# Kernel tuning notes

Hardware: AMD Instinct MI355X
Metric: run time of the kernel (lower is better)

The kernel has to match this reference:

```python
import jax, jax.numpy as jnp
import numpy as np

B, N, D, H = 4, 512, 4, 256


def _linear_params(key, fan_in, fan_out):
    # torch.nn.Linear default init: U(-1/sqrt(fan_in), 1/sqrt(fan_in))
    lim = 1.0 / np.sqrt(fan_in)
    kw, kb = jax.random.split(key)
    W = jax.random.uniform(kw, (fan_in, fan_out), minval=-lim, maxval=lim, dtype=jnp.float32)
    b = jax.random.uniform(kb, (fan_out,), minval=-lim, maxval=lim, dtype=jnp.float32)
    return W, b


def setup_inputs() -> dict:
    key = jax.random.key(0)
    ks = jax.random.split(key, 8)
    x = jax.random.normal(ks[0], (B, N, D), dtype=jnp.float32)
    adj = jax.random.uniform(ks[1], (B, N, N), dtype=jnp.float32)  # soft adjacency in [0,1)
    W_e1, b_e1 = _linear_params(ks[2], 2 * D, H)
    W_e2, b_e2 = _linear_params(ks[3], H, H)
    W_n1, b_n1 = _linear_params(ks[4], H, H)
    W_n2, b_n2 = _linear_params(ks[5], H, H)
    W_o1, b_o1 = _linear_params(ks[6], D + H, H)
    W_o, b_o = _linear_params(ks[7], H, D)
    return {
        "x": x, "adj": adj,
        "W_e1": W_e1, "b_e1": b_e1, "W_e2": W_e2, "b_e2": b_e2,
        "W_n1": W_n1, "b_n1": b_n1, "W_n2": W_n2, "b_n2": b_n2,
        "W_o1": W_o1, "b_o1": b_o1, "W_o": W_o, "b_o": b_o,
    }


def reference(x, adj, W_e1, b_e1, W_e2, b_e2, W_n1, b_n1, W_n2, b_n2, W_o1, b_o1, W_o, b_o):
    b_, n_, d_ = x.shape
    # innode[b,i,j,:] = x[b,j]; outnode[b,i,j,:] = x[b,i]
    innode = jnp.broadcast_to(x[:, None, :, :], (b_, n_, n_, d_))
    outnode = jnp.broadcast_to(x[:, :, None, :], (b_, n_, n_, d_))
    edge_in = jnp.concatenate([innode, outnode], axis=-1)          # [B,N,N,2D]
    node2edge = jax.nn.relu(edge_in @ W_e1 + b_e1)                 # [B,N,N,H]
    edge2edge = jax.nn.relu(node2edge @ W_e2 + b_e2)               # [B,N,N,H]
    # adjacency-masked sum over axis 1 (the i axis)
    agg = jnp.einsum('bij,bijh->bjh', adj, edge2edge)              # [B,N,H]
    out1 = jax.nn.relu(agg @ W_n1 + b_n1)
    out2 = jax.nn.relu(out1 @ W_n2 + b_n2)
    out3 = jnp.concatenate([x, out2], axis=-1)                     # [B,N,D+H]
    out4 = out3 @ W_o1 + b_o1
    out5 = out4 @ W_o + b_o                                        # [B,N,D]
    # CONTINUOUS is False for the classifier variant
    return jax.nn.log_softmax(out5, axis=2)
```

## Files before the change

kernel.cpp:

```cpp
#include <hip/hip_runtime.h>
#include <hip/hip_fp16.h>
#include <math.h>

#define Bq 4
#define Nq 512
#define Dq 4
#define Hq 256

typedef _Float16 f16x8 __attribute__((ext_vector_type(8)));
typedef float f32x4 __attribute__((ext_vector_type(4)));

__device__ __forceinline__ f16x8 hadd_relu(f16x8 u, f16x8 v) {
    f16x8 s = u + v;
    const f16x8 z = (f16x8)(_Float16)0.0f;
    return __builtin_elementwise_max(s, z);
}

__global__ __launch_bounds__(256) void prep_uv(
    const float* __restrict__ x, const float* __restrict__ We1,
    const float* __restrict__ be1, __half* __restrict__ U, __half* __restrict__ V) {
    const int bn = blockIdx.x;
    const int k = threadIdx.x;
    const float* xp = x + bn * Dq;
    const float x0 = xp[0], x1 = xp[1], x2 = xp[2], x3 = xp[3];
    float u = be1[k];
    u = fmaf(x0, We1[0 * 256 + k], u);
    u = fmaf(x1, We1[1 * 256 + k], u);
    u = fmaf(x2, We1[2 * 256 + k], u);
    u = fmaf(x3, We1[3 * 256 + k], u);
    float v = x0 * We1[4 * 256 + k];
    v = fmaf(x1, We1[5 * 256 + k], v);
    v = fmaf(x2, We1[6 * 256 + k], v);
    v = fmaf(x3, We1[7 * 256 + k], v);
    U[(size_t)bn * Hq + k] = __float2half(u);
    V[(size_t)bn * Hq + k] = __float2half(v);
}

__global__ __launch_bounds__(256, 2) void edge_gemm(
    const __half* __restrict__ U, const __half* __restrict__ V,
    const float* __restrict__ We2, const float* __restrict__ be2,
    const float* __restrict__ adj, float* __restrict__ aggws) {
    __shared__ __align__(16) char smem[59392];
    __half* Wt = (__half*)smem;
    __half* Us = (__half*)(smem + 32768);
    __half* Vs = (__half*)(smem + 40960);
    float* adjs = (float*)(smem + 57344);
    float* red = (float*)(smem + 40960);

    const int bid = blockIdx.x;
    const int hq_ = bid & 3;
    const int jt = (bid >> 2) & 31;
    const int b = bid >> 7;
    const int h_base = hq_ * 64;
    const int j_base = jt * 16;
    const int t = threadIdx.x;
    const int lane = t & 63;
    const int w = t >> 6;
    const int q = lane >> 4;
    const int l15 = lane & 15;

    const __half* Vb = V + (size_t)b * Nq * Hq;
    const float* adjb = adj + (size_t)b * Nq * Nq;

    const int srow = t >> 4;
    const int sc0 = (t & 15) * 2;

    {
        const int n = t & 63;
        const int swz = n & 31;
        for (int kk = (t >> 6); kk < 256; kk += 4) {
            float val = We2[kk * 256 + h_base + n];
            Wt[n * 256 + ((((kk >> 3) ^ swz)) << 3) + (kk & 7)] = __float2half(val);
        }
    }
    {
        const uint4* gp = (const uint4*)(U + (size_t)(b * Nq + j_base + srow) * Hq);
        uint4 v0 = gp[sc0];
        uint4 v1 = gp[sc0 + 1];
        *(uint4*)&Us[srow * 256 + ((sc0 ^ srow) << 3)] = v0;
        *(uint4*)&Us[srow * 256 + (((sc0 + 1) ^ srow) << 3)] = v1;
    }

    float bias[4];
#pragma unroll
    for (int nt = 0; nt < 4; ++nt) bias[nt] = be2[h_base + nt * 16 + l15];

    f32x4 agg[4];
#pragma unroll
    for (int nt = 0; nt < 4; ++nt) agg[nt] = (f32x4){0.f, 0.f, 0.f, 0.f};

    uint4 pva, pvb; float pad_;
    {
        const uint4* gp = (const uint4*)(Vb + (size_t)(0 + srow) * Hq);
        pva = gp[sc0]; pvb = gp[sc0 + 1];
        pad_ = adjb[(size_t)(0 + srow) * Nq + j_base + (t & 15)];
        *(uint4*)&Vs[0 * 4096 + srow * 256 + ((sc0 ^ srow) << 3)] = pva;
        *(uint4*)&Vs[0 * 4096 + srow * 256 + (((sc0 + 1) ^ srow) << 3)] = pvb;
        adjs[0 * 256 + t] = pad_;
    }
    {
        const uint4* gp = (const uint4*)(Vb + (size_t)(16 + srow) * Hq);
        pva = gp[sc0]; pvb = gp[sc0 + 1];
        pad_ = adjb[(size_t)(16 + srow) * Nq + j_base + (t & 15)];
    }
    __syncthreads();

    for (int ch = 0; ch < 32; ++ch) {
        const int cur = ch & 1;
        const __half* Vcur = Vs + cur * 4096;
        const float* Acur = adjs + cur * 256;

        f32x4 acc[4][4];
#pragma unroll
        for (int mi = 0; mi < 4; ++mi)
#pragma unroll
            for (int nt = 0; nt < 4; ++nt)
                acc[mi][nt] = (f32x4){bias[nt], bias[nt], bias[nt], bias[nt]};

#pragma unroll
        for (int ks = 0; ks < 8; ++ks) {
            const int c = ks * 4 + q;
            const f16x8 uvec = *(const f16x8*)&Us[l15 * 256 + ((c ^ l15) << 3)];
            f16x8 afrag[4];
#pragma unroll
            for (int mi = 0; mi < 4; ++mi) {
                const int iv = w * 4 + mi;
                const f16x8 vvec = *(const f16x8*)&Vcur[iv * 256 + ((c ^ iv) << 3)];
                afrag[mi] = hadd_relu(uvec, vvec);
            }
            f16x8 bf[4];
#pragma unroll
            for (int nt = 0; nt < 4; ++nt) {
                const int rn = nt * 16 + l15;
                bf[nt] = *(const f16x8*)&Wt[rn * 256 + ((c ^ (rn & 31)) << 3)];
            }
#pragma unroll
            for (int mi = 0; mi < 4; ++mi)
#pragma unroll
                for (int nt = 0; nt < 4; ++nt)
                    acc[mi][nt] = __builtin_amdgcn_mfma_f32_16x16x32_f16(
                        afrag[mi], bf[nt], acc[mi][nt], 0, 0, 0);
        }

#pragma unroll
        for (int mi = 0; mi < 4; ++mi) {
            const int iv = w * 4 + mi;
            const f32x4 av = *(const f32x4*)&Acur[iv * 16 + q * 4];
#pragma unroll
            for (int nt = 0; nt < 4; ++nt) {
                agg[nt][0] = fmaf(av[0], fmaxf(acc[mi][nt][0], 0.f), agg[nt][0]);
                agg[nt][1] = fmaf(av[1], fmaxf(acc[mi][nt][1], 0.f), agg[nt][1]);
                agg[nt][2] = fmaf(av[2], fmaxf(acc[mi][nt][2], 0.f), agg[nt][2]);
                agg[nt][3] = fmaf(av[3], fmaxf(acc[mi][nt][3], 0.f), agg[nt][3]);
            }
        }

        if (ch < 31) {
            const int nxt = cur ^ 1;
            *(uint4*)&Vs[nxt * 4096 + srow * 256 + ((sc0 ^ srow) << 3)] = pva;
            *(uint4*)&Vs[nxt * 4096 + srow * 256 + (((sc0 + 1) ^ srow) << 3)] = pvb;
            adjs[nxt * 256 + t] = pad_;
            if (ch < 30) {
                const int i_base = (ch + 2) * 16;
                const uint4* gp = (const uint4*)(Vb + (size_t)(i_base + srow) * Hq);
                pva = gp[sc0]; pvb = gp[sc0 + 1];
                pad_ = adjb[(size_t)(i_base + srow) * Nq + j_base + (t & 15)];
            }
        }
        __syncthreads();
    }

#pragma unroll
    for (int nt = 0; nt < 4; ++nt)
#pragma unroll
        for (int r = 0; r < 4; ++r)
            red[w * 1024 + (q * 4 + r) * 64 + nt * 16 + l15] = agg[nt][r];
    __syncthreads();
    {
        const int j = t >> 4;
        const int h0 = (t & 15) * 4;
        f32x4 s = *(const f32x4*)&red[0 * 1024 + j * 64 + h0];
        s += *(const f32x4*)&red[1 * 1024 + j * 64 + h0];
        s += *(const f32x4*)&red[2 * 1024 + j * 64 + h0];
        s += *(const f32x4*)&red[3 * 1024 + j * 64 + h0];
        *(f32x4*)&aggws[(size_t)(b * Nq + j_base + j) * Hq + h_base + h0] = s;
    }
}

__global__ __launch_bounds__(256) void tail_kernel(
    const float* __restrict__ aggws, const float* __restrict__ x,
    const float* __restrict__ Wn1, const float* __restrict__ bn1,
    const float* __restrict__ Wn2, const float* __restrict__ bn2,
    const float* __restrict__ Wo1, const float* __restrict__ bo1,
    const float* __restrict__ Wo, const float* __restrict__ bo,
    float* __restrict__ out) {
    __shared__ __align__(16) float bufA[256 * 4];
    __shared__ __align__(16) float bufB[256 * 4];
    __shared__ float xs[4][4];
    __shared__ float s5[4][4];
    const int bid = blockIdx.x;
    const int b = bid >> 7;
    const int n0 = (bid & 127) * 4;
    const int t = threadIdx.x;

#pragma unroll
    for (int ni = 0; ni < 4; ++ni)
        bufA[t * 4 + ni] = aggws[(size_t)(b * Nq + n0 + ni) * Hq + t];
    if (t < 16) xs[t >> 2][t & 3] = x[(size_t)(b * Nq + n0 + (t >> 2)) * Dq + (t & 3)];
    __syncthreads();

    float c0, c1, c2, c3;
    c0 = c1 = c2 = c3 = bn1[t];
#pragma unroll 8
    for (int k = 0; k < 256; ++k) {
        const float wv = Wn1[k * 256 + t];
        const float4 av = *(const float4*)&bufA[k * 4];
        c0 = fmaf(av.x, wv, c0); c1 = fmaf(av.y, wv, c1);
        c2 = fmaf(av.z, wv, c2); c3 = fmaf(av.w, wv, c3);
    }
    bufB[t * 4 + 0] = fmaxf(c0, 0.f); bufB[t * 4 + 1] = fmaxf(c1, 0.f);
    bufB[t * 4 + 2] = fmaxf(c2, 0.f); bufB[t * 4 + 3] = fmaxf(c3, 0.f);
    __syncthreads();

    c0 = c1 = c2 = c3 = bn2[t];
#pragma unroll 8
    for (int k = 0; k < 256; ++k) {
        const float wv = Wn2[k * 256 + t];
        const float4 av = *(const float4*)&bufB[k * 4];
        c0 = fmaf(av.x, wv, c0); c1 = fmaf(av.y, wv, c1);
        c2 = fmaf(av.z, wv, c2); c3 = fmaf(av.w, wv, c3);
    }
    bufA[t * 4 + 0] = fmaxf(c0, 0.f); bufA[t * 4 + 1] = fmaxf(c1, 0.f);
    bufA[t * 4 + 2] = fmaxf(c2, 0.f); bufA[t * 4 + 3] = fmaxf(c3, 0.f);
    __syncthreads();

    c0 = c1 = c2 = c3 = bo1[t];
#pragma unroll
    for (int d = 0; d < 4; ++d) {
        const float wv = Wo1[d * 256 + t];
        c0 = fmaf(xs[0][d], wv, c0); c1 = fmaf(xs[1][d], wv, c1);
        c2 = fmaf(xs[2][d], wv, c2); c3 = fmaf(xs[3][d], wv, c3);
    }
#pragma unroll 8
    for (int k = 0; k < 256; ++k) {
        const float wv = Wo1[(4 + k) * 256 + t];
        const float4 av = *(const float4*)&bufA[k * 4];
        c0 = fmaf(av.x, wv, c0); c1 = fmaf(av.y, wv, c1);
        c2 = fmaf(av.z, wv, c2); c3 = fmaf(av.w, wv, c3);
    }
    bufB[t * 4 + 0] = c0; bufB[t * 4 + 1] = c1;
    bufB[t * 4 + 2] = c2; bufB[t * 4 + 3] = c3;
    __syncthreads();

    const int d = t >> 6;
    const int lane = t & 63;
    float p0 = 0.f, p1 = 0.f, p2 = 0.f, p3 = 0.f;
    for (int k = lane; k < 256; k += 64) {
        const float wv = Wo[k * 4 + d];
        const float4 av = *(const float4*)&bufB[k * 4];
        p0 = fmaf(av.x, wv, p0); p1 = fmaf(av.y, wv, p1);
        p2 = fmaf(av.z, wv, p2); p3 = fmaf(av.w, wv, p3);
    }
#pragma unroll
    for (int off = 32; off > 0; off >>= 1) {
        p0 += __shfl_down(p0, off); p1 += __shfl_down(p1, off);
        p2 += __shfl_down(p2, off); p3 += __shfl_down(p3, off);
    }
    if (lane == 0) {
        s5[0][d] = p0 + bo[d]; s5[1][d] = p1 + bo[d];
        s5[2][d] = p2 + bo[d]; s5[3][d] = p3 + bo[d];
    }
    __syncthreads();
    if (t < 4) {
        const float v0 = s5[t][0], v1 = s5[t][1], v2 = s5[t][2], v3 = s5[t][3];
        const float m = fmaxf(fmaxf(v0, v1), fmaxf(v2, v3));
        const float s = expf(v0 - m) + expf(v1 - m) + expf(v2 - m) + expf(v3 - m);
        const float lse = m + logf(s);
        float* op = out + (size_t)(b * Nq + n0 + t) * Dq;
        op[0] = v0 - lse; op[1] = v1 - lse; op[2] = v2 - lse; op[3] = v3 - lse;
    }
}

extern "C" void kernel_launch(void* const* d_in, const int* in_sizes, int n_in,
                              void* d_out, int out_size, void* d_ws, size_t ws_size,
                              hipStream_t stream) {
    const float* x   = (const float*)d_in[0];
    const float* adj = (const float*)d_in[1];
    const float* We1 = (const float*)d_in[2];
    const float* be1 = (const float*)d_in[3];
    const float* We2 = (const float*)d_in[4];
    const float* be2 = (const float*)d_in[5];
    const float* Wn1 = (const float*)d_in[6];
    const float* bn1 = (const float*)d_in[7];
    const float* Wn2 = (const float*)d_in[8];
    const float* bn2 = (const float*)d_in[9];
    const float* Wo1 = (const float*)d_in[10];
    const float* bo1 = (const float*)d_in[11];
    const float* Wo  = (const float*)d_in[12];
    const float* bo  = (const float*)d_in[13];
    float* out = (float*)d_out;

    __half* U = (__half*)d_ws;
    __half* V = U + (size_t)Bq * Nq * Hq;
    float* aggws = (float*)((char*)d_ws + (size_t)2 * Bq * Nq * Hq * sizeof(__half));

    prep_uv<<<Bq * Nq, 256, 0, stream>>>(x, We1, be1, U, V);
    edge_gemm<<<512, 256, 0, stream>>>(U, V, We2, be2, adj, aggws);
    tail_kernel<<<512, 256, 0, stream>>>(aggws, x, Wn1, bn1, Wn2, bn2, Wo1, bo1, Wo, bo, out);
}
```

Baseline: 242.9 us.

## Split edge GEMM over i halves, keep U in registers, raise occupancy

The edge GEMM kernel now splits the i-reduction into two halves, doubling the grid to 1024 blocks. Each half writes its partial aggregate to a separate workspace slice, and the tail kernel sums the two slices. U fragments are held in registers instead of shared memory, which shrinks LDS use so launch bounds can request 3 blocks per SM. The aim is better occupancy and load balance across the CUs. The cost is twice the W staging per block, more registers per thread, and an extra partial-sum read in the tail.

```diff
diff --git a/kernel.cpp b/kernel.cpp
--- a/kernel.cpp
+++ b/kernel.cpp
@@ -36,23 +36,24 @@
     V[(size_t)bn * Hq + k] = __float2half(v);
 }
 
-__global__ __launch_bounds__(256, 2) void edge_gemm(
+__global__ __launch_bounds__(256, 3) void edge_gemm(
     const __half* __restrict__ U, const __half* __restrict__ V,
     const float* __restrict__ We2, const float* __restrict__ be2,
     const float* __restrict__ adj, float* __restrict__ aggws) {
-    __shared__ __align__(16) char smem[59392];
+    __shared__ __align__(16) char smem[51200];
     __half* Wt = (__half*)smem;
-    __half* Us = (__half*)(smem + 32768);
-    __half* Vs = (__half*)(smem + 40960);
-    float* adjs = (float*)(smem + 57344);
-    float* red = (float*)(smem + 40960);
+    __half* Vs = (__half*)(smem + 32768);
+    float* adjs = (float*)(smem + 49152);
+    float* red = (float*)(smem + 32768);
 
     const int bid = blockIdx.x;
     const int hq_ = bid & 3;
     const int jt = (bid >> 2) & 31;
-    const int b = bid >> 7;
+    const int ih = (bid >> 7) & 1;
+    const int b = bid >> 8;
     const int h_base = hq_ * 64;
     const int j_base = jt * 16;
+    const int i_first = ih * 256;
     const int t = threadIdx.x;
     const int lane = t & 63;
     const int w = t >> 6;
@@ -73,12 +74,12 @@
             Wt[n * 256 + ((((kk >> 3) ^ swz)) << 3) + (kk & 7)] = __float2half(val);
         }
     }
-    {
-        const uint4* gp = (const uint4*)(U + (size_t)(b * Nq + j_base + srow) * Hq);
-        uint4 v0 = gp[sc0];
-        uint4 v1 = gp[sc0 + 1];
-        *(uint4*)&Us[srow * 256 + ((sc0 ^ srow) << 3)] = v0;
-        *(uint4*)&Us[srow * 256 + (((sc0 + 1) ^ srow) << 3)] = v1;
+
+    f16x8 uvec[8];
+#pragma unroll
+    for (int ks = 0; ks < 8; ++ks) {
+        const int c = ks * 4 + q;
+        uvec[ks] = *(const f16x8*)&U[(size_t)(b * Nq + j_base + l15) * Hq + c * 8];
     }
 
     float bias[4];
@@ -91,21 +92,21 @@
 
     uint4 pva, pvb; float pad_;
     {
-        const uint4* gp = (const uint4*)(Vb + (size_t)(0 + srow) * Hq);
+        const uint4* gp = (const uint4*)(Vb + (size_t)(i_first + srow) * Hq);
         pva = gp[sc0]; pvb = gp[sc0 + 1];
-        pad_ = adjb[(size_t)(0 + srow) * Nq + j_base + (t & 15)];
+        pad_ = adjb[(size_t)(i_first + srow) * Nq + j_base + (t & 15)];
         *(uint4*)&Vs[0 * 4096 + srow * 256 + ((sc0 ^ srow) << 3)] = pva;
         *(uint4*)&Vs[0 * 4096 + srow * 256 + (((sc0 + 1) ^ srow) << 3)] = pvb;
         adjs[0 * 256 + t] = pad_;
     }
     {
-        const uint4* gp = (const uint4*)(Vb + (size_t)(16 + srow) * Hq);
+        const uint4* gp = (const uint4*)(Vb + (size_t)(i_first + 16 + srow) * Hq);
         pva = gp[sc0]; pvb = gp[sc0 + 1];
-        pad_ = adjb[(size_t)(16 + srow) * Nq + j_base + (t & 15)];
-    }
-    __syncthreads();
-
-    for (int ch = 0; ch < 32; ++ch) {
+        pad_ = adjb[(size_t)(i_first + 16 + srow) * Nq + j_base + (t & 15)];
+    }
+    __syncthreads();
+
+    for (int ch = 0; ch < 16; ++ch) {
         const int cur = ch & 1;
         const __half* Vcur = Vs + cur * 4096;
         const float* Acur = adjs + cur * 256;
@@ -120,13 +121,12 @@
 #pragma unroll
         for (int ks = 0; ks < 8; ++ks) {
             const int c = ks * 4 + q;
-            const f16x8 uvec = *(const f16x8*)&Us[l15 * 256 + ((c ^ l15) << 3)];
             f16x8 afrag[4];
 #pragma unroll
             for (int mi = 0; mi < 4; ++mi) {
                 const int iv = w * 4 + mi;
                 const f16x8 vvec = *(const f16x8*)&Vcur[iv * 256 + ((c ^ iv) << 3)];
-                afrag[mi] = hadd_relu(uvec, vvec);
+                afrag[mi] = hadd_relu(uvec[ks], vvec);
             }
             f16x8 bf[4];
 #pragma unroll
@@ -155,13 +155,13 @@
             }
         }
 
-        if (ch < 31) {
+        if (ch < 15) {
             const int nxt = cur ^ 1;
             *(uint4*)&Vs[nxt * 4096 + srow * 256 + ((sc0 ^ srow) << 3)] = pva;
             *(uint4*)&Vs[nxt * 4096 + srow * 256 + (((sc0 + 1) ^ srow) << 3)] = pvb;
             adjs[nxt * 256 + t] = pad_;
-            if (ch < 30) {
-                const int i_base = (ch + 2) * 16;
+            if (ch < 14) {
+                const int i_base = i_first + (ch + 2) * 16;
                 const uint4* gp = (const uint4*)(Vb + (size_t)(i_base + srow) * Hq);
                 pva = gp[sc0]; pvb = gp[sc0 + 1];
                 pad_ = adjb[(size_t)(i_base + srow) * Nq + j_base + (t & 15)];
@@ -183,7 +183,8 @@
         s += *(const f32x4*)&red[1 * 1024 + j * 64 + h0];
         s += *(const f32x4*)&red[2 * 1024 + j * 64 + h0];
         s += *(const f32x4*)&red[3 * 1024 + j * 64 + h0];
-        *(f32x4*)&aggws[(size_t)(b * Nq + j_base + j) * Hq + h_base + h0] = s;
+        float* aggp = aggws + (size_t)ih * Bq * Nq * Hq;
+        *(f32x4*)&aggp[(size_t)(b * Nq + j_base + j) * Hq + h_base + h0] = s;
     }
 }
 
@@ -203,9 +204,12 @@
     const int n0 = (bid & 127) * 4;
     const int t = threadIdx.x;
 
-#pragma unroll
-    for (int ni = 0; ni < 4; ++ni)
-        bufA[t * 4 + ni] = aggws[(size_t)(b * Nq + n0 + ni) * Hq + t];
+    const size_t half = (size_t)Bq * Nq * Hq;
+#pragma unroll
+    for (int ni = 0; ni < 4; ++ni) {
+        const size_t idx = (size_t)(b * Nq + n0 + ni) * Hq + t;
+        bufA[t * 4 + ni] = aggws[idx] + aggws[half + idx];
+    }
     if (t < 16) xs[t >> 2][t & 3] = x[(size_t)(b * Nq + n0 + (t >> 2)) * Dq + (t & 3)];
     __syncthreads();
 
@@ -305,6 +309,6 @@
     float* aggws = (float*)((char*)d_ws + (size_t)2 * Bq * Nq * Hq * sizeof(__half));
 
     prep_uv<<<Bq * Nq, 256, 0, stream>>>(x, We1, be1, U, V);
-    edge_gemm<<<512, 256, 0, stream>>>(U, V, We2, be2, adj, aggws);
+    edge_gemm<<<1024, 256, 0, stream>>>(U, V, We2, be2, adj, aggws);
     tail_kernel<<<512, 256, 0, stream>>>(aggws, x, Wn1, bn1, Wn2, bn2, Wo1, bo1, Wo, bo, out);
 }
```

New measurement: 536.0 us. 2.21x slower.

## Load V tiles directly into LDS asynchronously, double chunk size, widen tail rows

Applied to the files above, without the earlier changes.

The edge GEMM now streams V chunks straight from global memory into LDS with global_load_lds, instead of staging them through registers and doing swizzled LDS stores. Each chunk grows from 16 to 32 i-rows, which halves the number of barriers per block but doubles the accumulator registers. The LDS V tile is no longer XOR-swizzled, so bank conflicts may appear. Separately, the tail kernel handles 8 nodes per block instead of 4, reusing each weight load across more rows at the cost of half as many blocks.

```diff
diff --git a/kernel.cpp b/kernel.cpp
--- a/kernel.cpp
+++ b/kernel.cpp
@@ -14,6 +14,12 @@
     f16x8 s = u + v;
     const f16x8 z = (f16x8)(_Float16)0.0f;
     return __builtin_elementwise_max(s, z);
+}
+
+__device__ __forceinline__ void gl_lds16(const void* g, void* l) {
+    __builtin_amdgcn_global_load_lds(
+        (const __attribute__((address_space(1))) unsigned int*)g,
+        (__attribute__((address_space(3))) unsigned int*)l, 16, 0, 0);
 }
 
 __global__ __launch_bounds__(256) void prep_uv(
@@ -40,11 +46,11 @@
     const __half* __restrict__ U, const __half* __restrict__ V,
     const float* __restrict__ We2, const float* __restrict__ be2,
     const float* __restrict__ adj, float* __restrict__ aggws) {
-    __shared__ __align__(16) char smem[59392];
+    __shared__ __align__(16) char smem[77824];
     __half* Wt = (__half*)smem;
     __half* Us = (__half*)(smem + 32768);
     __half* Vs = (__half*)(smem + 40960);
-    float* adjs = (float*)(smem + 57344);
+    float* adjs = (float*)(smem + 73728);
     float* red = (float*)(smem + 40960);
 
     const int bid = blockIdx.x;
@@ -62,9 +68,6 @@
     const __half* Vb = V + (size_t)b * Nq * Hq;
     const float* adjb = adj + (size_t)b * Nq * Nq;
 
-    const int srow = t >> 4;
-    const int sc0 = (t & 15) * 2;
-
     {
         const int n = t & 63;
         const int swz = n & 31;
@@ -74,6 +77,8 @@
         }
     }
     {
+        const int srow = t >> 4;
+        const int sc0 = (t & 15) * 2;
         const uint4* gp = (const uint4*)(U + (size_t)(b * Nq + j_base + srow) * Hq);
         uint4 v0 = gp[sc0];
         uint4 v1 = gp[sc0 + 1];
@@ -89,30 +94,47 @@
 #pragma unroll
     for (int nt = 0; nt < 4; ++nt) agg[nt] = (f32x4){0.f, 0.f, 0.f, 0.f};
 
-    uint4 pva, pvb; float pad_;
+    const int r0 = t >> 4;
+    const int col = t & 15;
+
+#pragma unroll
+    for (int inst = 0; inst < 4; ++inst)
+        gl_lds16((const char*)Vb + (size_t)w * 4096 + inst * 1024 + lane * 16,
+                 Vs + w * 2048 + inst * 512);
     {
-        const uint4* gp = (const uint4*)(Vb + (size_t)(0 + srow) * Hq);
-        pva = gp[sc0]; pvb = gp[sc0 + 1];
-        pad_ = adjb[(size_t)(0 + srow) * Nq + j_base + (t & 15)];
-        *(uint4*)&Vs[0 * 4096 + srow * 256 + ((sc0 ^ srow) << 3)] = pva;
-        *(uint4*)&Vs[0 * 4096 + srow * 256 + (((sc0 + 1) ^ srow) << 3)] = pvb;
-        adjs[0 * 256 + t] = pad_;
-    }
-    {
-        const uint4* gp = (const uint4*)(Vb + (size_t)(16 + srow) * Hq);
-        pva = gp[sc0]; pvb = gp[sc0 + 1];
-        pad_ = adjb[(size_t)(16 + srow) * Nq + j_base + (t & 15)];
-    }
-    __syncthreads();
-
-    for (int ch = 0; ch < 32; ++ch) {
+        float a0 = adjb[(size_t)r0 * Nq + j_base + col];
+        float a1 = adjb[(size_t)(r0 + 16) * Nq + j_base + col];
+        adjs[t] = a0;
+        adjs[256 + t] = a1;
+    }
+    float pa0 = adjb[(size_t)(32 + r0) * Nq + j_base + col];
+    float pa1 = adjb[(size_t)(32 + r0 + 16) * Nq + j_base + col];
+    __syncthreads();
+
+    for (int ch = 0; ch < 16; ++ch) {
         const int cur = ch & 1;
-        const __half* Vcur = Vs + cur * 4096;
-        const float* Acur = adjs + cur * 256;
-
-        f32x4 acc[4][4];
-#pragma unroll
-        for (int mi = 0; mi < 4; ++mi)
+        const int nxt = cur ^ 1;
+        const __half* Vcur = Vs + cur * 8192;
+        const float* Acur = adjs + cur * 512;
+
+        if (ch < 15) {
+            const size_t goff = (size_t)(ch + 1) * 32 * 512;
+#pragma unroll
+            for (int inst = 0; inst < 4; ++inst)
+                gl_lds16((const char*)Vb + goff + (size_t)w * 4096 + inst * 1024 + lane * 16,
+                         Vs + nxt * 8192 + w * 2048 + inst * 512);
+            adjs[nxt * 512 + t] = pa0;
+            adjs[nxt * 512 + 256 + t] = pa1;
+            if (ch < 14) {
+                const int ib = (ch + 2) * 32;
+                pa0 = adjb[(size_t)(ib + r0) * Nq + j_base + col];
+                pa1 = adjb[(size_t)(ib + r0 + 16) * Nq + j_base + col];
+            }
+        }
+
+        f32x4 acc[8][4];
+#pragma unroll
+        for (int mi = 0; mi < 8; ++mi)
 #pragma unroll
             for (int nt = 0; nt < 4; ++nt)
                 acc[mi][nt] = (f32x4){bias[nt], bias[nt], bias[nt], bias[nt]};
@@ -121,13 +143,6 @@
         for (int ks = 0; ks < 8; ++ks) {
             const int c = ks * 4 + q;
             const f16x8 uvec = *(const f16x8*)&Us[l15 * 256 + ((c ^ l15) << 3)];
-            f16x8 afrag[4];
-#pragma unroll
-            for (int mi = 0; mi < 4; ++mi) {
-                const int iv = w * 4 + mi;
-                const f16x8 vvec = *(const f16x8*)&Vcur[iv * 256 + ((c ^ iv) << 3)];
-                afrag[mi] = hadd_relu(uvec, vvec);
-            }
             f16x8 bf[4];
 #pragma unroll
             for (int nt = 0; nt < 4; ++nt) {
@@ -135,16 +150,26 @@
                 bf[nt] = *(const f16x8*)&Wt[rn * 256 + ((c ^ (rn & 31)) << 3)];
             }
 #pragma unroll
-            for (int mi = 0; mi < 4; ++mi)
-#pragma unroll
-                for (int nt = 0; nt < 4; ++nt)
-                    acc[mi][nt] = __builtin_amdgcn_mfma_f32_16x16x32_f16(
-                        afrag[mi], bf[nt], acc[mi][nt], 0, 0, 0);
+            for (int g = 0; g < 2; ++g) {
+                f16x8 afrag[4];
+#pragma unroll
+                for (int m4 = 0; m4 < 4; ++m4) {
+                    const int iv = w * 8 + g * 4 + m4;
+                    const f16x8 vvec = *(const f16x8*)&Vcur[iv * 256 + c * 8];
+                    afrag[m4] = hadd_relu(uvec, vvec);
+                }
+#pragma unroll
+                for (int m4 = 0; m4 < 4; ++m4)
+#pragma unroll
+                    for (int nt = 0; nt < 4; ++nt)
+                        acc[g * 4 + m4][nt] = __builtin_amdgcn_mfma_f32_16x16x32_f16(
+                            afrag[m4], bf[nt], acc[g * 4 + m4][nt], 0, 0, 0);
+            }
         }
 
 #pragma unroll
-        for (int mi = 0; mi < 4; ++mi) {
-            const int iv = w * 4 + mi;
+        for (int mi = 0; mi < 8; ++mi) {
+            const int iv = w * 8 + mi;
             const f32x4 av = *(const f32x4*)&Acur[iv * 16 + q * 4];
 #pragma unroll
             for (int nt = 0; nt < 4; ++nt) {
@@ -152,19 +177,6 @@
                 agg[nt][1] = fmaf(av[1], fmaxf(acc[mi][nt][1], 0.f), agg[nt][1]);
                 agg[nt][2] = fmaf(av[2], fmaxf(acc[mi][nt][2], 0.f), agg[nt][2]);
                 agg[nt][3] = fmaf(av[3], fmaxf(acc[mi][nt][3], 0.f), agg[nt][3]);
-            }
-        }
-
-        if (ch < 31) {
-            const int nxt = cur ^ 1;
-            *(uint4*)&Vs[nxt * 4096 + srow * 256 + ((sc0 ^ srow) << 3)] = pva;
-            *(uint4*)&Vs[nxt * 4096 + srow * 256 + (((sc0 + 1) ^ srow) << 3)] = pvb;
-            adjs[nxt * 256 + t] = pad_;
-            if (ch < 30) {
-                const int i_base = (ch + 2) * 16;
-                const uint4* gp = (const uint4*)(Vb + (size_t)(i_base + srow) * Hq);
-                pva = gp[sc0]; pvb = gp[sc0 + 1];
-                pad_ = adjb[(size_t)(i_base + srow) * Nq + j_base + (t & 15)];
             }
         }
         __syncthreads();
@@ -194,84 +206,100 @@
     const float* __restrict__ Wo1, const float* __restrict__ bo1,
     const float* __restrict__ Wo, const float* __restrict__ bo,
     float* __restrict__ out) {
-    __shared__ __align__(16) float bufA[256 * 4];
-    __shared__ __align__(16) float bufB[256 * 4];
-    __shared__ float xs[4][4];
-    __shared__ float s5[4][4];
+    __shared__ __align__(16) float bufA[256 * 8];
+    __shared__ __align__(16) float bufB[256 * 8];
+    __shared__ float xs[8][4];
+    __shared__ float s5[8][4];
     const int bid = blockIdx.x;
-    const int b = bid >> 7;
-    const int n0 = (bid & 127) * 4;
+    const int b = bid >> 6;
+    const int n0 = (bid & 63) * 8;
     const int t = threadIdx.x;
 
 #pragma unroll
-    for (int ni = 0; ni < 4; ++ni)
-        bufA[t * 4 + ni] = aggws[(size_t)(b * Nq + n0 + ni) * Hq + t];
-    if (t < 16) xs[t >> 2][t & 3] = x[(size_t)(b * Nq + n0 + (t >> 2)) * Dq + (t & 3)];
-    __syncthreads();
-
-    float c0, c1, c2, c3;
-    c0 = c1 = c2 = c3 = bn1[t];
-#pragma unroll 8
+    for (int ni = 0; ni < 8; ++ni)
+        bufA[t * 8 + ni] = aggws[(size_t)(b * Nq + n0 + ni) * Hq + t];
+    if (t < 32) xs[t >> 2][t & 3] = x[(size_t)(b * Nq + n0 + (t >> 2)) * Dq + (t & 3)];
+    __syncthreads();
+
+    float c[8];
+#pragma unroll
+    for (int ni = 0; ni < 8; ++ni) c[ni] = bn1[t];
+#pragma unroll 4
     for (int k = 0; k < 256; ++k) {
         const float wv = Wn1[k * 256 + t];
-        const float4 av = *(const float4*)&bufA[k * 4];
-        c0 = fmaf(av.x, wv, c0); c1 = fmaf(av.y, wv, c1);
-        c2 = fmaf(av.z, wv, c2); c3 = fmaf(av.w, wv, c3);
-    }
-    bufB[t * 4 + 0] = fmaxf(c0, 0.f); bufB[t * 4 + 1] = fmaxf(c1, 0.f);
-    bufB[t * 4 + 2] = fmaxf(c2, 0.f); bufB[t * 4 + 3] = fmaxf(c3, 0.f);
-    __syncthreads();
-
-    c0 = c1 = c2 = c3 = bn2[t];
-#pragma unroll 8
+        const float4 a0 = *(const float4*)&bufA[k * 8];
+        const float4 a1 = *(const float4*)&bufA[k * 8 + 4];
+        c[0] = fmaf(a0.x, wv, c[0]); c[1] = fmaf(a0.y, wv, c[1]);
+        c[2] = fmaf(a0.z, wv, c[2]); c[3] = fmaf(a0.w, wv, c[3]);
+        c[4] = fmaf(a1.x, wv, c[4]); c[5] = fmaf(a1.y, wv, c[5]);
+        c[6] = fmaf(a1.z, wv, c[6]); c[7] = fmaf(a1.w, wv, c[7]);
+    }
+#pragma unroll
+    for (int ni = 0; ni < 8; ++ni) bufB[t * 8 + ni] = fmaxf(c[ni], 0.f);
+    __syncthreads();
+
+#pragma unroll
+    for (int ni = 0; ni < 8; ++ni) c[ni] = bn2[t];
+#pragma unroll 4
     for (int k = 0; k < 256; ++k) {
         const float wv = Wn2[k * 256 + t];
-        const float4 av = *(const float4*)&bufB[k * 4];
-        c0 = fmaf(av.x, wv, c0); c1 = fmaf(av.y, wv, c1);
-        c2 = fmaf(av.z, wv, c2); c3 = fmaf(av.w, wv, c3);
-    }
-    bufA[t * 4 + 0] = fmaxf(c0, 0.f); bufA[t * 4 + 1] = fmaxf(c1, 0.f);
-    bufA[t * 4 + 2] = fmaxf(c2, 0.f); bufA[t * 4 + 3] = fmaxf(c3, 0.f);
-    __syncthreads();
-
-    c0 = c1 = c2 = c3 = bo1[t];
+        const float4 a0 = *(const float4*)&bufB[k * 8];
+        const float4 a1 = *(const float4*)&bufB[k * 8 + 4];
+        c[0] = fmaf(a0.x, wv, c[0]); c[1] = fmaf(a0.y, wv, c[1]);
+        c[2] = fmaf(a0.z, wv, c[2]); c[3] = fmaf(a0.w, wv, c[3]);
+        c[4] = fmaf(a1.x, wv, c[4]); c[5] = fmaf(a1.y, wv, c[5]);
+        c[6] = fmaf(a1.z, wv, c[6]); c[7] = fmaf(a1.w, wv, c[7]);
+    }
+#pragma unroll
+    for (int ni = 0; ni < 8; ++ni) bufA[t * 8 + ni] = fmaxf(c[ni], 0.f);
+    __syncthreads();
+
+#pragma unroll
+    for (int ni = 0; ni < 8; ++ni) c[ni] = bo1[t];
 #pragma unroll
     for (int d = 0; d < 4; ++d) {
         const float wv = Wo1[d * 256 + t];
-        c0 = fmaf(xs[0][d], wv, c0); c1 = fmaf(xs[1][d], wv, c1);
-        c2 = fmaf(xs[2][d], wv, c2); c3 = fmaf(xs[3][d], wv, c3);
-    }
-#pragma unroll 8
+#pragma unroll
+        for (int ni = 0; ni < 8; ++ni) c[ni] = fmaf(xs[ni][d], wv, c[ni]);
+    }
+#pragma unroll 4
     for (int k = 0; k < 256; ++k) {
         const float wv = Wo1[(4 + k) * 256 + t];
-        const float4 av = *(const float4*)&bufA[k * 4];
-        c0 = fmaf(av.x, wv, c0); c1 = fmaf(av.y, wv, c1);
-        c2 = fmaf(av.z, wv, c2); c3 = fmaf(av.w, wv, c3);
-    }
-    bufB[t * 4 + 0] = c0; bufB[t * 4 + 1] = c1;
-    bufB[t * 4 + 2] = c2; bufB[t * 4 + 3] = c3;
+        const float4 a0 = *(const float4*)&bufA[k * 8];
+        const float4 a1 = *(const float4*)&bufA[k * 8 + 4];
+        c[0] = fmaf(a0.x, wv, c[0]); c[1] = fmaf(a0.y, wv, c[1]);
+        c[2] = fmaf(a0.z, wv, c[2]); c[3] = fmaf(a0.w, wv, c[3]);
+        c[4] = fmaf(a1.x, wv, c[4]); c[5] = fmaf(a1.y, wv, c[5]);
+        c[6] = fmaf(a1.z, wv, c[6]); c[7] = fmaf(a1.w, wv, c[7]);
+    }
+#pragma unroll
+    for (int ni = 0; ni < 8; ++ni) bufB[t * 8 + ni] = c[ni];
     __syncthreads();
 
     const int d = t >> 6;
     const int lane = t & 63;
-    float p0 = 0.f, p1 = 0.f, p2 = 0.f, p3 = 0.f;
+    float p[8];
+#pragma unroll
+    for (int ni = 0; ni < 8; ++ni) p[ni] = 0.f;
     for (int k = lane; k < 256; k += 64) {
         const float wv = Wo[k * 4 + d];
-        const float4 av = *(const float4*)&bufB[k * 4];
-        p0 = fmaf(av.x, wv, p0); p1 = fmaf(av.y, wv, p1);
-        p2 = fmaf(av.z, wv, p2); p3 = fmaf(av.w, wv, p3);
-    }
-#pragma unroll
-    for (int off = 32; off > 0; off >>= 1) {
-        p0 += __shfl_down(p0, off); p1 += __shfl_down(p1, off);
-        p2 += __shfl_down(p2, off); p3 += __shfl_down(p3, off);
-    }
+        const float4 a0 = *(const float4*)&bufB[k * 8];
+        const float4 a1 = *(const float4*)&bufB[k * 8 + 4];
+        p[0] = fmaf(a0.x, wv, p[0]); p[1] = fmaf(a0.y, wv, p[1]);
+        p[2] = fmaf(a0.z, wv, p[2]); p[3] = fmaf(a0.w, wv, p[3]);
+        p[4] = fmaf(a1.x, wv, p[4]); p[5] = fmaf(a1.y, wv, p[5]);
+        p[6] = fmaf(a1.z, wv, p[6]); p[7] = fmaf(a1.w, wv, p[7]);
+    }
+#pragma unroll
+    for (int off = 32; off > 0; off >>= 1)
+#pragma unroll
+        for (int ni = 0; ni < 8; ++ni) p[ni] += __shfl_down(p[ni], off);
     if (lane == 0) {
-        s5[0][d] = p0 + bo[d]; s5[1][d] = p1 + bo[d];
-        s5[2][d] = p2 + bo[d]; s5[3][d] = p3 + bo[d];
-    }
-    __syncthreads();
-    if (t < 4) {
+#pragma unroll
+        for (int ni = 0; ni < 8; ++ni) s5[ni][d] = p[ni] + bo[d];
+    }
+    __syncthreads();
+    if (t < 8) {
         const float v0 = s5[t][0], v1 = s5[t][1], v2 = s5[t][2], v3 = s5[t][3];
         const float m = fmaxf(fmaxf(v0, v1), fmaxf(v2, v3));
         const float s = expf(v0 - m) + expf(v1 - m) + expf(v2 - m) + expf(v3 - m);
@@ -306,5 +334,5 @@
 
     prep_uv<<<Bq * Nq, 256, 0, stream>>>(x, We1, be1, U, V);
     edge_gemm<<<512, 256, 0, stream>>>(U, V, We2, be2, adj, aggws);
-    tail_kernel<<<512, 256, 0, stream>>>(aggws, x, Wn1, bn1, Wn2, bn2, Wo1, bo1, Wo, bo, out);
-}
+    tail_kernel<<<256, 256, 0, stream>>>(aggws, x, Wn1, bn1, Wn2, bn2, Wo1, bo1, Wo, bo, out);
+}
```

Measured after the change: 283.8 us. 1.17x slower.

## Rewrite node MLP tail with fp16 MFMA over 64-row tiles

Applied to the files above, without the earlier changes.

Replaces the scalar fp32 tail kernel, which handled 4 nodes per block, with an MFMA-based version that handles 64 nodes per block using fp16 activations in swizzled shared memory. A new wprep kernel transposes and converts Wn1, Wn2 and Wo1 to fp16 each call. The goal is to stop re-streaming the 256x256 fp32 weights for every 4 nodes and to use matrix cores. In exchange it adds a kernel launch, lowers precision to fp16, and runs the tail on only 32 blocks, so much of the GPU sits idle.

```diff
diff --git a/kernel.cpp b/kernel.cpp
--- a/kernel.cpp
+++ b/kernel.cpp
@@ -14,6 +14,13 @@
     f16x8 s = u + v;
     const f16x8 z = (f16x8)(_Float16)0.0f;
     return __builtin_elementwise_max(s, z);
+}
+
+__device__ __forceinline__ uint4 cvt8h(const float* p) {
+    union { __half h[8]; uint4 u; } r;
+#pragma unroll
+    for (int i = 0; i < 8; ++i) r.h[i] = __float2half(p[i]);
+    return r.u;
 }
 
 __global__ __launch_bounds__(256) void prep_uv(
@@ -36,6 +43,16 @@
     V[(size_t)bn * Hq + k] = __float2half(v);
 }
 
+__global__ __launch_bounds__(256) void wprep(
+    const float* __restrict__ Wn1, const float* __restrict__ Wn2,
+    const float* __restrict__ Wo1, __half* __restrict__ Wt16) {
+    const int n = blockIdx.x & 255;
+    const int mat = blockIdx.x >> 8;
+    const int k = threadIdx.x;
+    const float* W = (mat == 0) ? Wn1 : (mat == 1) ? Wn2 : (Wo1 + 4 * 256);
+    Wt16[((size_t)mat * 256 + n) * 256 + k] = __float2half(W[k * 256 + n]);
+}
+
 __global__ __launch_bounds__(256, 2) void edge_gemm(
     const __half* __restrict__ U, const __half* __restrict__ V,
     const float* __restrict__ We2, const float* __restrict__ be2,
@@ -187,96 +204,143 @@
     }
 }
 
+__device__ __forceinline__ void mlp_layer_relu(
+    const __half* actIn, __half* actOut, const __half* __restrict__ Wt,
+    const float* __restrict__ bias, int w, int q, int l15) {
+    f32x4 acc[16];
+#pragma unroll
+    for (int nt = 0; nt < 16; ++nt) {
+        const float bv = bias[nt * 16 + l15];
+        acc[nt] = (f32x4){bv, bv, bv, bv};
+    }
+#pragma unroll
+    for (int ks = 0; ks < 8; ++ks) {
+        const int c = ks * 4 + q;
+        const f16x8 af = *(const f16x8*)&actIn[(w * 16 + l15) * 256 + ((c ^ l15) << 3)];
+#pragma unroll
+        for (int nt = 0; nt < 16; ++nt) {
+            const f16x8 bf = *(const f16x8*)&Wt[(size_t)(nt * 16 + l15) * 256 + c * 8];
+            acc[nt] = __builtin_amdgcn_mfma_f32_16x16x32_f16(af, bf, acc[nt], 0, 0, 0);
+        }
+    }
+#pragma unroll
+    for (int nt = 0; nt < 16; ++nt) {
+        const int n = nt * 16 + l15;
+        const int g = n >> 3;
+#pragma unroll
+        for (int r = 0; r < 4; ++r) {
+            const int row = w * 16 + q * 4 + r;
+            actOut[row * 256 + ((g ^ (row & 15)) << 3) + (n & 7)] =
+                __float2half(fmaxf(acc[nt][r], 0.f));
+        }
+    }
+}
+
 __global__ __launch_bounds__(256) void tail_kernel(
     const float* __restrict__ aggws, const float* __restrict__ x,
-    const float* __restrict__ Wn1, const float* __restrict__ bn1,
-    const float* __restrict__ Wn2, const float* __restrict__ bn2,
+    const __half* __restrict__ Wt16,
+    const float* __restrict__ bn1, const float* __restrict__ bn2,
     const float* __restrict__ Wo1, const float* __restrict__ bo1,
     const float* __restrict__ Wo, const float* __restrict__ bo,
     float* __restrict__ out) {
-    __shared__ __align__(16) float bufA[256 * 4];
-    __shared__ __align__(16) float bufB[256 * 4];
-    __shared__ float xs[4][4];
-    __shared__ float s5[4][4];
-    const int bid = blockIdx.x;
-    const int b = bid >> 7;
-    const int n0 = (bid & 127) * 4;
+    __shared__ __align__(16) __half actA[64 * 256];
+    __shared__ __align__(16) __half actB[64 * 256];
+    __shared__ float xs[64][4];
+    __shared__ float s5[64][4];
+    const int g0 = blockIdx.x * 64;
     const int t = threadIdx.x;
-
-#pragma unroll
-    for (int ni = 0; ni < 4; ++ni)
-        bufA[t * 4 + ni] = aggws[(size_t)(b * Nq + n0 + ni) * Hq + t];
-    if (t < 16) xs[t >> 2][t & 3] = x[(size_t)(b * Nq + n0 + (t >> 2)) * Dq + (t & 3)];
-    __syncthreads();
-
-    float c0, c1, c2, c3;
-    c0 = c1 = c2 = c3 = bn1[t];
-#pragma unroll 8
-    for (int k = 0; k < 256; ++k) {
-        const float wv = Wn1[k * 256 + t];
-        const float4 av = *(const float4*)&bufA[k * 4];
-        c0 = fmaf(av.x, wv, c0); c1 = fmaf(av.y, wv, c1);
-        c2 = fmaf(av.z, wv, c2); c3 = fmaf(av.w, wv, c3);
-    }
-    bufB[t * 4 + 0] = fmaxf(c0, 0.f); bufB[t * 4 + 1] = fmaxf(c1, 0.f);
-    bufB[t * 4 + 2] = fmaxf(c2, 0.f); bufB[t * 4 + 3] = fmaxf(c3, 0.f);
-    __syncthreads();
-
-    c0 = c1 = c2 = c3 = bn2[t];
-#pragma unroll 8
-    for (int k = 0; k < 256; ++k) {
-        const float wv = Wn2[k * 256 + t];
-        const float4 av = *(const float4*)&bufB[k * 4];
-        c0 = fmaf(av.x, wv, c0); c1 = fmaf(av.y, wv, c1);
-        c2 = fmaf(av.z, wv, c2); c3 = fmaf(av.w, wv, c3);
-    }
-    bufA[t * 4 + 0] = fmaxf(c0, 0.f); bufA[t * 4 + 1] = fmaxf(c1, 0.f);
-    bufA[t * 4 + 2] = fmaxf(c2, 0.f); bufA[t * 4 + 3] = fmaxf(c3, 0.f);
-    __syncthreads();
-
-    c0 = c1 = c2 = c3 = bo1[t];
-#pragma unroll
-    for (int d = 0; d < 4; ++d) {
-        const float wv = Wo1[d * 256 + t];
-        c0 = fmaf(xs[0][d], wv, c0); c1 = fmaf(xs[1][d], wv, c1);
-        c2 = fmaf(xs[2][d], wv, c2); c3 = fmaf(xs[3][d], wv, c3);
-    }
-#pragma unroll 8
-    for (int k = 0; k < 256; ++k) {
-        const float wv = Wo1[(4 + k) * 256 + t];
-        const float4 av = *(const float4*)&bufA[k * 4];
-        c0 = fmaf(av.x, wv, c0); c1 = fmaf(av.y, wv, c1);
-        c2 = fmaf(av.z, wv, c2); c3 = fmaf(av.w, wv, c3);
-    }
-    bufB[t * 4 + 0] = c0; bufB[t * 4 + 1] = c1;
-    bufB[t * 4 + 2] = c2; bufB[t * 4 + 3] = c3;
-    __syncthreads();
-
-    const int d = t >> 6;
     const int lane = t & 63;
-    float p0 = 0.f, p1 = 0.f, p2 = 0.f, p3 = 0.f;
-    for (int k = lane; k < 256; k += 64) {
-        const float wv = Wo[k * 4 + d];
-        const float4 av = *(const float4*)&bufB[k * 4];
-        p0 = fmaf(av.x, wv, p0); p1 = fmaf(av.y, wv, p1);
-        p2 = fmaf(av.z, wv, p2); p3 = fmaf(av.w, wv, p3);
-    }
-#pragma unroll
-    for (int off = 32; off > 0; off >>= 1) {
-        p0 += __shfl_down(p0, off); p1 += __shfl_down(p1, off);
-        p2 += __shfl_down(p2, off); p3 += __shfl_down(p3, off);
-    }
-    if (lane == 0) {
-        s5[0][d] = p0 + bo[d]; s5[1][d] = p1 + bo[d];
-        s5[2][d] = p2 + bo[d]; s5[3][d] = p3 + bo[d];
-    }
-    __syncthreads();
-    if (t < 4) {
+    const int w = t >> 6;
+    const int q = lane >> 4;
+    const int l15 = lane & 15;
+
+    {
+        const int row = t >> 2;
+        const int cb = (t & 3) * 8;
+        const float* src = aggws + (size_t)(g0 + row) * 256 + cb * 8;
+#pragma unroll
+        for (int g = 0; g < 8; ++g) {
+            const int c = cb + g;
+            *(uint4*)&actA[row * 256 + ((c ^ (row & 15)) << 3)] = cvt8h(src + g * 8);
+        }
+    }
+    if (t < 64) {
+        const float4 xv = *(const float4*)&x[(size_t)(g0 + t) * 4];
+        xs[t][0] = xv.x; xs[t][1] = xv.y; xs[t][2] = xv.z; xs[t][3] = xv.w;
+    }
+    __syncthreads();
+
+    mlp_layer_relu(actA, actB, Wt16 + 0 * 65536, bn1, w, q, l15);
+    __syncthreads();
+    mlp_layer_relu(actB, actA, Wt16 + 1 * 65536, bn2, w, q, l15);
+    __syncthreads();
+
+    f32x4 acc[16];
+#pragma unroll
+    for (int nt = 0; nt < 16; ++nt) {
+        const int n = nt * 16 + l15;
+        const float bv = bo1[n];
+        const float w0 = Wo1[0 * 256 + n], w1 = Wo1[1 * 256 + n];
+        const float w2 = Wo1[2 * 256 + n], w3 = Wo1[3 * 256 + n];
+#pragma unroll
+        for (int r = 0; r < 4; ++r) {
+            const int row = w * 16 + q * 4 + r;
+            float v = bv;
+            v = fmaf(xs[row][0], w0, v); v = fmaf(xs[row][1], w1, v);
+            v = fmaf(xs[row][2], w2, v); v = fmaf(xs[row][3], w3, v);
+            acc[nt][r] = v;
+        }
+    }
+#pragma unroll
+    for (int ks = 0; ks < 8; ++ks) {
+        const int c = ks * 4 + q;
+        const f16x8 af = *(const f16x8*)&actA[(w * 16 + l15) * 256 + ((c ^ l15) << 3)];
+#pragma unroll
+        for (int nt = 0; nt < 16; ++nt) {
+            const f16x8 bf = *(const f16x8*)&Wt16[(size_t)2 * 65536 + (size_t)(nt * 16 + l15) * 256 + c * 8];
+            acc[nt] = __builtin_amdgcn_mfma_f32_16x16x32_f16(af, bf, acc[nt], 0, 0, 0);
+        }
+    }
+
+    float p[4][4];
+#pragma unroll
+    for (int r = 0; r < 4; ++r)
+#pragma unroll
+        for (int d = 0; d < 4; ++d) p[r][d] = 0.f;
+#pragma unroll
+    for (int nt = 0; nt < 16; ++nt) {
+        const int n = nt * 16 + l15;
+        const float4 wv = *(const float4*)&Wo[n * 4];
+#pragma unroll
+        for (int r = 0; r < 4; ++r) {
+            p[r][0] = fmaf(acc[nt][r], wv.x, p[r][0]);
+            p[r][1] = fmaf(acc[nt][r], wv.y, p[r][1]);
+            p[r][2] = fmaf(acc[nt][r], wv.z, p[r][2]);
+            p[r][3] = fmaf(acc[nt][r], wv.w, p[r][3]);
+        }
+    }
+#pragma unroll
+    for (int off = 1; off < 16; off <<= 1)
+#pragma unroll
+        for (int r = 0; r < 4; ++r)
+#pragma unroll
+            for (int d = 0; d < 4; ++d)
+                p[r][d] += __shfl_xor(p[r][d], off);
+    if (l15 == 0) {
+#pragma unroll
+        for (int r = 0; r < 4; ++r) {
+            const int row = w * 16 + q * 4 + r;
+#pragma unroll
+            for (int d = 0; d < 4; ++d) s5[row][d] = p[r][d] + bo[d];
+        }
+    }
+    __syncthreads();
+    if (t < 64) {
         const float v0 = s5[t][0], v1 = s5[t][1], v2 = s5[t][2], v3 = s5[t][3];
         const float m = fmaxf(fmaxf(v0, v1), fmaxf(v2, v3));
         const float s = expf(v0 - m) + expf(v1 - m) + expf(v2 - m) + expf(v3 - m);
         const float lse = m + logf(s);
-        float* op = out + (size_t)(b * Nq + n0 + t) * Dq;
+        float* op = out + (size_t)(g0 + t) * 4;
         op[0] = v0 - lse; op[1] = v1 - lse; op[2] = v2 - lse; op[3] = v3 - lse;
     }
 }
@@ -303,8 +367,10 @@
     __half* U = (__half*)d_ws;
     __half* V = U + (size_t)Bq * Nq * Hq;
     float* aggws = (float*)((char*)d_ws + (size_t)2 * Bq * Nq * Hq * sizeof(__half));
+    __half* Wt16 = (__half*)((char*)d_ws + (size_t)4 * 1024 * 1024);
 
     prep_uv<<<Bq * Nq, 256, 0, stream>>>(x, We1, be1, U, V);
+    wprep<<<768, 256, 0, stream>>>(Wn1, Wn2, Wo1, Wt16);
     edge_gemm<<<512, 256, 0, stream>>>(U, V, We2, be2, adj, aggws);
-    tail_kernel<<<512, 256, 0, stream>>>(aggws, x, Wn1, bn1, Wn2, bn2, Wo1, bo1, Wo, bo, out);
-}
+    tail_kernel<<<32, 256, 0, stream>>>(aggws, x, Wt16, bn1, bn2, Wo1, bo1, Wo, bo, out);
+}
```

Measured after the change: 288.4 us. 1.19x slower.
